# Performance work log

Measured on AMD Instinct MI355X. Metric: run time of the kernel, lower is better.

Reference implementation:

```python
import jax, jax.numpy as jnp
import numpy as np

N_TBINS = 1024
K = 8
B = 32768
IRF_SIGMA = 10.0
PEAK_FACTOR = 5.0
# IRF1DLayer: circular pad (pad_l=N//2, pad_r=N//2-1 for even N) then conv1d with
# flip(irf)  ==  circular convolution with irf followed by roll of -(N-1-N//2).
ROLL_C = N_TBINS - 1 - N_TBINS // 2  # 511


def _wrapped_gaussian(n, mu, sigma):
    # circ_shifted gaussian pulse: wrap tails around the domain, normalize to unit area
    t = np.arange(n, dtype=np.float64)
    g = np.zeros(n, dtype=np.float64)
    for s in (-n, 0, n):
        g += np.exp(-((t - mu + s) ** 2) / (2.0 * sigma ** 2))
    g /= g.sum()
    return jnp.asarray(g, dtype=jnp.float32)


def _circ_conv(x, irf):
    # faithful IRF1DLayer: circular convolution, recentered
    y = jnp.fft.irfft(jnp.fft.rfft(x, axis=-1) * jnp.fft.rfft(irf), n=N_TBINS, axis=-1)
    return jnp.roll(y, -ROLL_C, axis=-1)


def setup_inputs():
    key = jax.random.key(0)
    k1, k2, k3, k4 = jax.random.split(key, 4)
    illumination = _wrapped_gaussian(N_TBINS, N_TBINS // 2, 30.0)  # Gaussian1DLayer buffer
    irf = _wrapped_gaussian(N_TBINS, (N_TBINS - 1) // 2, IRF_SIGMA)
    photon_counts = jax.random.uniform(k1, (B,), jnp.float32, 10.0, 1000.0)
    sbrs = jax.random.uniform(k2, (B,), jnp.float32, 0.1, 1.0)
    bins = jax.random.randint(k3, (B,), 0, N_TBINS)
    cmat_weight = jax.random.normal(k4, (K, N_TBINS), jnp.float32) * 0.05  # Conv1d(k, n_tbins, 1) weight
    return {"illumination": illumination, "photon_counts": photon_counts,
            "sbrs": sbrs, "irf": irf, "cmat_weight": cmat_weight, "bins": bins}


def reference(illumination, photon_counts, sbrs, irf, cmat_weight, bins):
    n = N_TBINS
    inp = _circ_conv(jax.nn.relu(illumination), irf)          # [N] = irf(relu(illum))
    shifts = (bins % n).astype(jnp.int32)                     # [B]
    amb_per_bin = (photon_counts / sbrs) / n                  # [B]
    area = jnp.sum(inp)                                       # current_area
    scale = photon_counts / area                              # [B]
    scaled = inp[None, :] * scale[:, None]                    # [B, N]
    clamped = jnp.minimum(scaled, (PEAK_FACTOR * photon_counts)[:, None])
    offset = clamped + amb_per_bin[:, None]                   # [B, N]
    conv = _circ_conv(offset, irf)                            # [B, N] (batched FFT conv)
    # torch.roll(x, s): out[t] = x[(t - s) % N], vectorized over batch
    idx = (jnp.arange(n)[None, :] - shifts[:, None]) % n      # [B, N]
    shifted = jnp.take_along_axis(conv, idx, axis=1)          # [B, N]
    rate = jax.lax.stop_gradient(shifted)                     # torch.poisson detaches
    noisy = jax.random.poisson(jax.random.key(42), rate, shape=rate.shape).astype(jnp.float32)
    # cmat1D: Conv1d(in=n_tbins, out=k, kernel=1) on [B, N, 1] -> [B, K, 1]
    out = jnp.einsum('bn,kn->bk', noisy, cmat_weight)[..., None]
    return out
```

## Files before the change

kernel.cpp:

```cpp
#include <hip/hip_runtime.h>
#include <hip/hip_bf16.h>
#include <stdint.h>

#define N_T   1024
#define ROLLC 511
#define KCH   8
#define KN_LEV 48
#define DENSE_L 3
#define RJ_LEV 24
#define CH_N  (2*KN_LEV + 4*RJ_LEV)

__device__ double   g_inp[N_T];
__device__ double   g_conv2[N_T];
__device__ double   g_area;
__device__ uint32_t g_chains[CH_N];
__device__ int      g_T;
__device__ float    g_ll5, g_aa5, g_bb5, g_inva5, g_vr5;

struct TF2 { uint32_t x, y; };

__device__ __forceinline__ TF2 tf2x32(uint32_t k0, uint32_t k1, uint32_t c0, uint32_t c1) {
  uint32_t ks2 = k0 ^ k1 ^ 0x1BD11BDAu;
  uint32_t x0 = c0 + k0, x1 = c1 + k1;
#define TFR(r) { x0 += x1; x1 = (x1 << (r)) | (x1 >> (32 - (r))); x1 ^= x0; }
  TFR(13) TFR(15) TFR(26) TFR(6)
  x0 += k1;  x1 += ks2 + 1u;
  TFR(17) TFR(29) TFR(16) TFR(24)
  x0 += ks2; x1 += k0 + 2u;
  TFR(13) TFR(15) TFR(26) TFR(6)
  x0 += k0;  x1 += k1 + 3u;
  TFR(17) TFR(29) TFR(16) TFR(24)
  x0 += k1;  x1 += ks2 + 4u;
  TFR(13) TFR(15) TFR(26) TFR(6)
  x0 += ks2; x1 += k0 + 5u;
#undef TFR
  return {x0, x1};
}

__device__ __forceinline__ float u01_from_key(uint32_t sk0, uint32_t sk1, uint32_t m) {
  TF2 r = tf2x32(sk0, sk1, 0u, m);
  uint32_t bits = r.x ^ r.y;
  return __uint_as_float((bits >> 9) | 0x3f800000u) - 1.0f;
}

__device__ __forceinline__ float lgamma_xla(float x) {
#pragma clang fp contract(off)
  float z = x - 1.0f;
  float sum = 1.0f;
  sum = sum + 676.5203681218851f     / (z + 1.0f);
  sum = sum + -1259.1392167224028f   / (z + 2.0f);
  sum = sum + 771.32342877765313f    / (z + 3.0f);
  sum = sum + -176.61502916214059f   / (z + 4.0f);
  sum = sum + 12.507343278686905f    / (z + 5.0f);
  sum = sum + -0.13857109526572012f  / (z + 6.0f);
  sum = sum + 9.9843695780195716e-6f / (z + 7.0f);
  sum = sum + 1.5056327351493116e-7f / (z + 8.0f);
  float t = 7.5f + z;
  float log_t = 2.0149030205422647f + log1pf(z / 7.5f);
  return 0.91893853320467274f + (z + 0.5f - t / log_t) * log_t + logf(sum);
}

__device__ __forceinline__ void rej_constants(float lam, float* ll, float* aa, float* bb,
                                              float* inva, float* vr) {
#pragma clang fp contract(off)
  *ll = logf(lam);
  float b = 0.931f + 2.53f * sqrtf(lam);
  float a = -0.059f + 0.02483f * b;
  *bb = b; *aa = a;
  *inva = 1.1239f + 1.1328f / (b - 3.4f);
  *vr = 0.9277f - 3.6224f / (b - 2.0f);
}

__device__ __forceinline__ int ptrs_quick(float lamr, float aa, float bb, float vr,
                                          float u, float v) {
#pragma clang fp contract(off)
  float us = 0.5f - fabsf(u);
  float kf = floorf((2.0f * aa / us + bb) * u + lamr + 0.43f);
  if ((us >= 0.07f) && (v <= vr)) return 1;
  if ((kf < 0.0f) || ((us < 0.013f) && (v > us))) return -1;
  return 0;
}

__device__ __forceinline__ bool ptrs_slow(float lamr, float ll, float aa, float bb,
                                          float inva, float u, float v) {
#pragma clang fp contract(off)
  float us = 0.5f - fabsf(u);
  float kf = floorf((2.0f * aa / us + bb) * u + lamr + 0.43f);
  float s = logf(v * inva / (aa / (us * us) + bb));
  float t = (-lamr + kf * ll) - lgamma_xla(kf + 1.0f);
  return s <= t;
}

__device__ __forceinline__ bool rej_iter(float lam, float ll, float aa, float bb,
                                         float inva, float vr, float u, float v, float* kf) {
#pragma clang fp contract(off)
  float us = 0.5f - fabsf(u);
  float k = floorf((2.0f * aa / us + bb) * u + lam + 0.43f);
  *kf = k;
  if ((us >= 0.07f) && (v <= vr)) return true;
  if ((k < 0.0f) || ((us < 0.013f) && (v > us))) return false;
  float s = logf(v * inva / (aa / (us * us) + bb));
  float t = (-lam + k * ll) - lgamma_xla(k + 1.0f);
  return s <= t;
}

__device__ __forceinline__ uint32_t wave_append(bool pred, uint32_t* counter) {
  unsigned long long vote = __ballot(pred);
  int lane = threadIdx.x & 63;
  uint32_t base = 0;
  int cnt = __popcll(vote);
  if (cnt) {
    int leader = __ffsll((unsigned long long)vote) - 1;
    if (lane == leader) base = atomicAdd(counter, (uint32_t)cnt);
    base = (uint32_t)__shfl((int)base, leader, 64);
  }
  return base + (uint32_t)__popcll(vote & ((1ull << lane) - 1ull));
}

__global__ void __launch_bounds__(128)
pre1_kernel(const float* __restrict__ illum, const float* __restrict__ irf) {
  __shared__ double xs[N_T], irfs[N_T];
  const int tid = threadIdx.x;
  for (int i = tid; i < N_T; i += 128) {
    xs[i]   = fmax((double)illum[i], 0.0);
    irfs[i] = (double)irf[i];
  }
  __syncthreads();
  const int t  = blockIdx.x * 128 + tid;
  const int tt = (t + ROLLC) & (N_T - 1);
  double acc = 0.0;
  for (int j = 0; j < N_T; ++j) acc += xs[j] * irfs[(tt - j) & (N_T - 1)];
  g_inp[t] = acc;
}

__global__ void __launch_bounds__(128)
pre2_kernel(const float* __restrict__ irf, uint32_t* __restrict__ wcount) {
  __shared__ double inps[N_T], irfs[N_T];
  const int tid = threadIdx.x;
  if (blockIdx.x < 8) {
    for (int i = tid; i < N_T; i += 128) {
      inps[i] = g_inp[i];
      irfs[i] = (double)irf[i];
    }
    __syncthreads();
    const int t  = blockIdx.x * 128 + tid;
    const int tt = (t + ROLLC) & (N_T - 1);
    double acc = 0.0;
    for (int j = 0; j < N_T; ++j) acc += inps[j] * irfs[(tt - j) & (N_T - 1)];
    g_conv2[t] = acc;
  } else {
    if (tid == 0) {
      g_T = 1;
      wcount[0] = 0u;
      double area = 0.0;
      for (int j = 0; j < N_T; ++j) area += g_inp[j];
      g_area = area;
    } else if (tid == 1) {
      uint32_t r0 = 0u, r1 = 42u;
      for (int j = 0; j < KN_LEV; ++j) {
        TF2 sub = tf2x32(r0, r1, 0u, 1u);
        TF2 nxt = tf2x32(r0, r1, 0u, 0u);
        g_chains[2*j] = sub.x; g_chains[2*j+1] = sub.y;
        r0 = nxt.x; r1 = nxt.y;
      }
    } else if (tid == 2) {
      uint32_t c0 = 0u, c1 = 42u;
      for (int j = 0; j < RJ_LEV; ++j) {
        TF2 nxt = tf2x32(c0, c1, 0u, 0u);
        TF2 s0  = tf2x32(c0, c1, 0u, 1u);
        TF2 s1  = tf2x32(c0, c1, 0u, 2u);
        int base = 2*KN_LEV + 4*j;
        g_chains[base]   = s0.x; g_chains[base+1] = s0.y;
        g_chains[base+2] = s1.x; g_chains[base+3] = s1.y;
        c0 = nxt.x; c1 = nxt.y;
      }
    } else if (tid == 3) {
      float ll, aa, bb, inva, vr;
      rej_constants(1e5f, &ll, &aa, &bb, &inva, &vr);
      g_ll5 = ll; g_aa5 = aa; g_bb5 = bb; g_inva5 = inva; g_vr5 = vr;
    }
  }
}

__global__ void __launch_bounds__(256)
t1_kernel(const float* __restrict__ photon, const float* __restrict__ sbr,
          const int* __restrict__ bins, uint32_t* __restrict__ wcount,
          uint2* __restrict__ recs, uint32_t cap) {
  __shared__ uint2    lrec[N_T];
  __shared__ uint32_t amb_m[N_T];
  __shared__ float    amb_u[N_T], amb_v[N_T], amb_lam[N_T];
  __shared__ uint32_t lcount, acount, gbase;
  const int b = blockIdx.x, tid = threadIdx.x;
  if (tid == 0) { lcount = 0u; acount = 0u; }
  __syncthreads();

  const float ph = photon[b], sb = sbr[b];
  const int   shift = bins[b] & (N_T - 1);
  const double scale = (double)ph / g_area;
  const float  r1f = ph / sb;
  const double amb = (double)r1f * (1.0 / 1024.0);
  const uint32_t sa0 = g_chains[2*KN_LEV+0], sa1 = g_chains[2*KN_LEV+1];
  const uint32_t sc0 = g_chains[2*KN_LEV+2], sc1 = g_chains[2*KN_LEV+3];
  const float ll5 = g_ll5, aa5 = g_aa5, bb5 = g_bb5, inva5 = g_inva5, vr5 = g_vr5;
  const uint32_t mbase = (uint32_t)b << 10;

  for (int i2 = 0; i2 < 4; ++i2) {
    const int t   = tid + (i2 << 8);
    const int src = (t - shift) & (N_T - 1);
    const float lam = (float)(scale * g_conv2[src] + amb);
    float lamr, aa, bbv, vr;
    if (lam < 10.0f) { lamr = 1e5f; aa = aa5; bbv = bb5; vr = vr5; }
    else {
#pragma clang fp contract(off)
      lamr = lam;
      float b2 = 0.931f + 2.53f * sqrtf(lam);
      bbv = b2; aa = -0.059f + 0.02483f * b2;
      vr = 0.9277f - 3.6224f / (b2 - 2.0f);
    }
    const uint32_t m = mbase + (uint32_t)t;
    float u = u01_from_key(sa0, sa1, m) - 0.5f;
    float v = u01_from_key(sc0, sc1, m);
    int cls = ptrs_quick(lamr, aa, bbv, vr, u, v);
    bool surv = (cls < 0);
    bool ambg = (cls == 0);
    uint32_t sS = wave_append(surv, &lcount);
    if (surv) lrec[sS] = make_uint2(m, __float_as_uint(lamr));
    uint32_t sA = wave_append(ambg, &acount);
    if (ambg) { amb_m[sA] = m; amb_u[sA] = u; amb_v[sA] = v; amb_lam[sA] = lamr; }
  }
  __syncthreads();

  const uint32_t na = acount;
  const uint32_t naPad = (na + 255u) & ~255u;
  for (uint32_t i = tid; i < naPad; i += 256) {
    bool active = (i < na);
    bool surv = false;
    uint32_t m = 0; float lamr = 0.f;
    if (active) {
      m = amb_m[i]; lamr = amb_lam[i];
      float u = amb_u[i], v = amb_v[i];
      float ll, aa, bbv, inva;
      if (lamr == 1e5f) { ll = ll5; aa = aa5; bbv = bb5; inva = inva5; }
      else {
#pragma clang fp contract(off)
        float b2 = 0.931f + 2.53f * sqrtf(lamr);
        bbv = b2; aa = -0.059f + 0.02483f * b2;
        ll = logf(lamr);
        inva = 1.1239f + 1.1328f / (b2 - 3.4f);
      }
      surv = !ptrs_slow(lamr, ll, aa, bbv, inva, u, v);
    }
    uint32_t sS = wave_append(surv, &lcount);
    if (surv) lrec[sS] = make_uint2(m, __float_as_uint(lamr));
  }
  __syncthreads();

  if (tid == 0) gbase = atomicAdd(wcount, lcount);
  __syncthreads();
  const uint32_t lc = lcount, base = gbase;
  for (uint32_t i = tid; i < lc; i += 256) {
    const uint32_t g = base + i;
    uint2 r = lrec[i];
    if (g < cap) {
      recs[g] = r;
    } else {
      const uint32_t m = r.x; const float lamr = __uint_as_float(r.y);
      float ll, aaf, bbf, invaf, vrf;
      if (lamr == 1e5f) { ll = ll5; aaf = aa5; bbf = bb5; invaf = inva5; vrf = vr5; }
      else rej_constants(lamr, &ll, &aaf, &bbf, &invaf, &vrf);
      int jf = RJ_LEV;
#pragma unroll 1
      for (int j = 1; j < RJ_LEV; ++j) {
        const uint32_t* c = g_chains + 2*KN_LEV + 4*j;
        float uu = u01_from_key(c[0], c[1], m) - 0.5f;
        float vv = u01_from_key(c[2], c[3], m);
        float kk;
        if (rej_iter(lamr, ll, aaf, bbf, invaf, vrf, uu, vv, &kk)) { jf = j + 1; break; }
      }
      atomicMax(&g_T, jf);
    }
  }
}

__global__ void __launch_bounds__(256)
t2_kernel(const uint32_t* __restrict__ wcount, const uint2* __restrict__ recs, uint32_t cap) {
  __shared__ uint32_t chs[4*RJ_LEV];
  __shared__ int bmax;
  const int tid = threadIdx.x;
  if (tid < 4*RJ_LEV) chs[tid] = g_chains[2*KN_LEV + tid];
  if (tid == 0) bmax = 1;
  __syncthreads();
  uint32_t n = *wcount; if (n > cap) n = cap;
  const float ll5 = g_ll5, aa5 = g_aa5, bb5 = g_bb5, inva5 = g_inva5, vr5 = g_vr5;
  int mymax = 1;
  for (uint32_t gi = blockIdx.x * 256u + tid; gi < n; gi += gridDim.x * 256u) {
    uint2 r = recs[gi];
    const uint32_t m = r.x; const float lamr = __uint_as_float(r.y);
    float ll, aa, bbv, inva, vr;
    if (lamr == 1e5f) { ll = ll5; aa = aa5; bbv = bb5; inva = inva5; vr = vr5; }
    else rej_constants(lamr, &ll, &aa, &bbv, &inva, &vr);
    int jf = RJ_LEV;
#pragma unroll 1
    for (int j = 1; j < RJ_LEV; ++j) {
      float uu = u01_from_key(chs[4*j], chs[4*j+1], m) - 0.5f;
      float vv = u01_from_key(chs[4*j+2], chs[4*j+3], m);
      float kk;
      if (rej_iter(lamr, ll, aa, bbv, inva, vr, uu, vv, &kk)) { jf = j + 1; break; }
    }
    mymax = max(mymax, jf);
  }
  for (int off = 32; off > 0; off >>= 1) mymax = max(mymax, __shfl_down(mymax, off, 64));
  if ((tid & 63) == 0) atomicMax(&bmax, mymax);
  __syncthreads();
  if (tid == 0) atomicMax(&g_T, bmax);
}

__global__ void __launch_bounds__(256)
sample_kernel(const float* __restrict__ photon, const float* __restrict__ sbr,
              const int* __restrict__ bins, const float* __restrict__ w,
              float* __restrict__ out) {
  __shared__ uint32_t ch[CH_N];
  __shared__ float lamS[N_T];
  __shared__ float cntS[N_T];
  __shared__ uint16_t rejL[N_T];
  __shared__ uint16_t surPK[N_T];
  __shared__ float    surLP[N_T];
  __shared__ uint32_t nSur, nRej;
  __shared__ float wred[4][KCH];
  const int b = blockIdx.x, tid = threadIdx.x;
  if (tid < CH_N) ch[tid] = g_chains[tid];
  if (tid == 0) { nSur = 0u; nRej = 0u; }
  __syncthreads();

  const float ph = photon[b], sb = sbr[b];
  const int   shift = bins[b] & (N_T - 1);
  const double scale = (double)ph / g_area;
  const float  r1f = ph / sb;
  const double amb = (double)r1f * (1.0 / 1024.0);
  const uint32_t mbase = (uint32_t)b << 10;

  for (int i2 = 0; i2 < 4; ++i2) {
    const int t   = tid + (i2 << 8);
    const int src = (t - shift) & (N_T - 1);
    const float lam = (float)(scale * g_conv2[src] + amb);
    lamS[t] = lam;
    const bool kn = (lam < 10.0f);
    const float neg = -lam;
    const uint32_t m = mbase + (uint32_t)t;
    float lp = 0.0f; int k = 0;
#pragma unroll
    for (int j = 0; j < DENSE_L; ++j) {
      k += (lp > neg) ? 1 : 0;
      float u = u01_from_key(ch[2*j], ch[2*j+1], m);
      lp += __logf(u);
    }
    const bool alive = (lp > neg);
    if (kn && !alive) cntS[t] = (float)(k - 1);
    bool srv = kn && alive;
    uint32_t sS = wave_append(srv, &nSur);
    if (srv) { surPK[sS] = (uint16_t)((k << 10) | t); surLP[sS] = lp; }
    uint32_t sR = wave_append(!kn, &nRej);
    if (!kn) rejL[sR] = (uint16_t)t;
  }
  __syncthreads();

  {
    const uint32_t nS = nSur;
    for (uint32_t i = tid; i < nS; i += 256) {
      const uint16_t pk = surPK[i];
      const uint16_t t16 = pk & 1023u;
      int k = pk >> 10;
      float lp = surLP[i];
      const float neg = -lamS[t16];
      const uint32_t m = mbase + (uint32_t)t16;
      int j = DENSE_L;
#pragma unroll 1
      while ((lp > neg) && (j < KN_LEV)) {
        ++k;
        lp += __logf(u01_from_key(ch[2*j], ch[2*j+1], m));
        ++j;
      }
      cntS[t16] = (float)(k - 1);
    }
  }

  {
    const int T = g_T;
    const uint32_t nr = nRej;
    for (uint32_t i = tid; i < nr; i += 256) {
      const uint16_t t16 = rejL[i];
      const float lam = lamS[t16];
      const uint32_t m = mbase + (uint32_t)t16;
      float ll, aa, bbv, inva, vr;
      rej_constants(lam, &ll, &aa, &bbv, &inva, &vr);
      float kout = -1.0f;
#pragma unroll 1
      for (int j = T - 1; j >= 0; --j) {
        const uint32_t* c = ch + 2*KN_LEV + 4*j;
        float u = u01_from_key(c[0], c[1], m) - 0.5f;
        float v = u01_from_key(c[2], c[3], m);
        float kf;
        if (rej_iter(lam, ll, aa, bbv, inva, vr, u, v, &kf)) { kout = kf; break; }
      }
      cntS[t16] = kout;
    }
  }
  __syncthreads();

  float acc[KCH];
#pragma unroll
  for (int k = 0; k < KCH; ++k) acc[k] = 0.0f;
  for (int i2 = 0; i2 < 4; ++i2) {
    const int t = tid + (i2 << 8);
    const float c = cntS[t];
#pragma unroll
    for (int k = 0; k < KCH; ++k) acc[k] += c * w[k * N_T + t];
  }
  const int lane = tid & 63, wv = tid >> 6;
#pragma unroll
  for (int k = 0; k < KCH; ++k) {
    float v = acc[k];
    for (int off = 32; off > 0; off >>= 1) v += __shfl_down(v, off, 64);
    if (lane == 0) wred[wv][k] = v;
  }
  __syncthreads();
  if (tid < KCH)
    out[b * KCH + tid] = wred[0][tid] + wred[1][tid] + wred[2][tid] + wred[3][tid];
}

extern "C" void kernel_launch(void* const* d_in, const int* in_sizes, int n_in,
                              void* d_out, int out_size, void* d_ws, size_t ws_size,
                              hipStream_t stream) {
  (void)n_in; (void)out_size;
  const float* illum  = (const float*)d_in[0];
  const float* photon = (const float*)d_in[1];
  const float* sbr    = (const float*)d_in[2];
  const float* irf    = (const float*)d_in[3];
  const float* w      = (const float*)d_in[4];
  const int*   bins   = (const int*)d_in[5];
  float* out = (float*)d_out;
  const int B = in_sizes[1];

  uint32_t* wcount = (uint32_t*)d_ws;
  uint2*    recs   = (uint2*)((char*)d_ws + 16);
  uint32_t  cap    = (ws_size > 16) ? (uint32_t)((ws_size - 16) / sizeof(uint2)) : 0u;

  pre1_kernel<<<8, 128, 0, stream>>>(illum, irf);
  pre2_kernel<<<9, 128, 0, stream>>>(irf, wcount);
  t1_kernel<<<B, 256, 0, stream>>>(photon, sbr, bins, wcount, recs, cap);
  t2_kernel<<<2048, 256, 0, stream>>>(wcount, recs, cap);
  sample_kernel<<<B, 256, 0, stream>>>(photon, sbr, bins, w, out);
}
```

Baseline: 1.137 ms.

## Fuse Knuth Poisson sampling into first pass and slim rejection-only second pass

The Knuth small-lambda sampling and its partial dot products move into the first per-batch kernel, which also does the PTRS quick/slow classification. The ambiguous slow test now runs inline instead of through a separate compaction pass. Shared-memory append counters are replaced with per-wave register counters and wave-local staging, and the dense Knuth depth is sized adaptively from the wave's maximum lambda. The final kernel only handles rejection-sampled bins, with the loop unrolled by four, and atomically adds to the output, returning early when a block has none. This removes one full pass over lambda and several block barriers, at the cost of more divergence and more register pressure in the fused kernel.

```diff
diff --git a/kernel.cpp b/kernel.cpp
--- a/kernel.cpp
+++ b/kernel.cpp
@@ -6,7 +6,6 @@
 #define ROLLC 511
 #define KCH   8
 #define KN_LEV 48
-#define DENSE_L 3
 #define RJ_LEV 24
 #define CH_N  (2*KN_LEV + 4*RJ_LEV)
 
@@ -102,19 +101,6 @@
   float s = logf(v * inva / (aa / (us * us) + bb));
   float t = (-lam + k * ll) - lgamma_xla(k + 1.0f);
   return s <= t;
-}
-
-__device__ __forceinline__ uint32_t wave_append(bool pred, uint32_t* counter) {
-  unsigned long long vote = __ballot(pred);
-  int lane = threadIdx.x & 63;
-  uint32_t base = 0;
-  int cnt = __popcll(vote);
-  if (cnt) {
-    int leader = __ffsll((unsigned long long)vote) - 1;
-    if (lane == leader) base = atomicAdd(counter, (uint32_t)cnt);
-    base = (uint32_t)__shfl((int)base, leader, 64);
-  }
-  return base + (uint32_t)__popcll(vote & ((1ull << lane) - 1ull));
 }
 
 __global__ void __launch_bounds__(128)
@@ -183,84 +169,146 @@
 }
 
 __global__ void __launch_bounds__(256)
-t1_kernel(const float* __restrict__ photon, const float* __restrict__ sbr,
-          const int* __restrict__ bins, uint32_t* __restrict__ wcount,
+kA_kernel(const float* __restrict__ photon, const float* __restrict__ sbr,
+          const int* __restrict__ bins, const float* __restrict__ w,
+          float* __restrict__ out, uint32_t* __restrict__ wcount,
           uint2* __restrict__ recs, uint32_t cap) {
-  __shared__ uint2    lrec[N_T];
-  __shared__ uint32_t amb_m[N_T];
-  __shared__ float    amb_u[N_T], amb_v[N_T], amb_lam[N_T];
-  __shared__ uint32_t lcount, acount, gbase;
+  __shared__ uint32_t ch[CH_N];
+  __shared__ uint2    sstage[N_T];
+  __shared__ uint16_t tpk[N_T];
+  __shared__ float    tlp[N_T];
+  __shared__ uint32_t scnts[4];
+  __shared__ uint32_t sbase;
+  __shared__ float    wred[4][KCH];
   const int b = blockIdx.x, tid = threadIdx.x;
-  if (tid == 0) { lcount = 0u; acount = 0u; }
-  __syncthreads();
-
-  const float ph = photon[b], sb = sbr[b];
-  const int   shift = bins[b] & (N_T - 1);
+  const int wv = tid >> 6, lane = tid & 63;
+  for (int i = tid; i < CH_N; i += 256) ch[i] = g_chains[i];
+  __syncthreads();
+
+  const float  ph = photon[b], sb = sbr[b];
+  const int    shift = bins[b] & (N_T - 1);
   const double scale = (double)ph / g_area;
   const float  r1f = ph / sb;
   const double amb = (double)r1f * (1.0 / 1024.0);
-  const uint32_t sa0 = g_chains[2*KN_LEV+0], sa1 = g_chains[2*KN_LEV+1];
-  const uint32_t sc0 = g_chains[2*KN_LEV+2], sc1 = g_chains[2*KN_LEV+3];
+  const uint32_t mbase = (uint32_t)b << 10;
+  const uint32_t ka0 = ch[2*KN_LEV+0], ka1 = ch[2*KN_LEV+1];
+  const uint32_t kc0 = ch[2*KN_LEV+2], kc1 = ch[2*KN_LEV+3];
   const float ll5 = g_ll5, aa5 = g_aa5, bb5 = g_bb5, inva5 = g_inva5, vr5 = g_vr5;
-  const uint32_t mbase = (uint32_t)b << 10;
+  const unsigned long long lmask = (1ull << lane) - 1ull;
+
+  uint32_t wcS = 0;
+  uint32_t wcT = 0;
+  float acc[KCH];
+#pragma unroll
+  for (int k = 0; k < KCH; ++k) acc[k] = 0.0f;
 
   for (int i2 = 0; i2 < 4; ++i2) {
-    const int t   = tid + (i2 << 8);
+    const int t   = (wv << 8) + (i2 << 6) + lane;
     const int src = (t - shift) & (N_T - 1);
     const float lam = (float)(scale * g_conv2[src] + amb);
-    float lamr, aa, bbv, vr;
-    if (lam < 10.0f) { lamr = 1e5f; aa = aa5; bbv = bb5; vr = vr5; }
-    else {
-#pragma clang fp contract(off)
-      lamr = lam;
-      float b2 = 0.931f + 2.53f * sqrtf(lam);
-      bbv = b2; aa = -0.059f + 0.02483f * b2;
-      vr = 0.9277f - 3.6224f / (b2 - 2.0f);
-    }
-    const uint32_t m = mbase + (uint32_t)t;
-    float u = u01_from_key(sa0, sa1, m) - 0.5f;
-    float v = u01_from_key(sc0, sc1, m);
-    int cls = ptrs_quick(lamr, aa, bbv, vr, u, v);
-    bool surv = (cls < 0);
-    bool ambg = (cls == 0);
-    uint32_t sS = wave_append(surv, &lcount);
-    if (surv) lrec[sS] = make_uint2(m, __float_as_uint(lamr));
-    uint32_t sA = wave_append(ambg, &acount);
-    if (ambg) { amb_m[sA] = m; amb_u[sA] = u; amb_v[sA] = v; amb_lam[sA] = lamr; }
-  }
-  __syncthreads();
-
-  const uint32_t na = acount;
-  const uint32_t naPad = (na + 255u) & ~255u;
-  for (uint32_t i = tid; i < naPad; i += 256) {
-    bool active = (i < na);
-    bool surv = false;
-    uint32_t m = 0; float lamr = 0.f;
-    if (active) {
-      m = amb_m[i]; lamr = amb_lam[i];
-      float u = amb_u[i], v = amb_v[i];
-      float ll, aa, bbv, inva;
-      if (lamr == 1e5f) { ll = ll5; aa = aa5; bbv = bb5; inva = inva5; }
-      else {
-#pragma clang fp contract(off)
-        float b2 = 0.931f + 2.53f * sqrtf(lamr);
-        bbv = b2; aa = -0.059f + 0.02483f * b2;
-        ll = logf(lamr);
-        inva = 1.1239f + 1.1328f / (b2 - 3.4f);
+    const bool  isRej = (lam >= 10.0f);
+    const float lamr  = isRej ? lam : 1e5f;
+    const uint32_t m  = mbase + (uint32_t)t;
+
+    float u = u01_from_key(ka0, ka1, m) - 0.5f;
+    float v = u01_from_key(kc0, kc1, m);
+    float bbq, aaq, vrq;
+    {
+#pragma clang fp contract(off)
+      float b2 = 0.931f + 2.53f * sqrtf(lamr);
+      float aq = -0.059f + 0.02483f * b2;
+      float vq = 0.9277f - 3.6224f / (b2 - 2.0f);
+      bbq = isRej ? b2 : bb5;
+      aaq = isRej ? aq : aa5;
+      vrq = isRej ? vq : vr5;
+    }
+    int cls = ptrs_quick(lamr, aaq, bbq, vrq, u, v);
+    bool surv;
+    if (cls == 0) {
+      float ll   = isRej ? logf(lamr) : ll5;
+      float inva;
+      {
+#pragma clang fp contract(off)
+        inva = isRej ? (1.1239f + 1.1328f / (bbq - 3.4f)) : inva5;
       }
-      surv = !ptrs_slow(lamr, ll, aa, bbv, inva, u, v);
-    }
-    uint32_t sS = wave_append(surv, &lcount);
-    if (surv) lrec[sS] = make_uint2(m, __float_as_uint(lamr));
-  }
-  __syncthreads();
-
-  if (tid == 0) gbase = atomicAdd(wcount, lcount);
-  __syncthreads();
-  const uint32_t lc = lcount, base = gbase;
-  for (uint32_t i = tid; i < lc; i += 256) {
+      surv = !ptrs_slow(lamr, ll, aaq, bbq, inva, u, v);
+    } else {
+      surv = (cls < 0);
+    }
+    {
+      unsigned long long vote = __ballot(surv);
+      uint32_t slot = wcS + (uint32_t)__popcll(vote & lmask);
+      if (surv) sstage[(wv << 8) + slot] = make_uint2(m, __float_as_uint(lamr));
+      wcS += (uint32_t)__popcll(vote);
+    }
+
+    const bool kn = !isRej;
+    const float neg = kn ? -lam : 1.0f;
+    float glam = kn ? lam : 0.0f;
+#pragma unroll
+    for (int off = 32; off > 0; off >>= 1) glam = fmaxf(glam, __shfl_xor(glam, off, 64));
+    int D = 0;
+    if (glam > 0.0f) {
+      D = (int)(glam + 2.0f * sqrtf(glam)) + 2;
+      if (D > KN_LEV) D = KN_LEV;
+    }
+    float lp = 0.0f; int k = 0;
+    for (int j = 0; j < D; ++j) {
+      k += (lp > neg) ? 1 : 0;
+      lp += __logf(u01_from_key(ch[2*j], ch[2*j+1], m));
+    }
+    const bool alive = kn && (lp > neg);
+    const float cntf = (kn && !alive) ? (float)(k - 1) : 0.0f;
+#pragma unroll
+    for (int kk = 0; kk < KCH; ++kk) acc[kk] += cntf * w[kk * N_T + t];
+    {
+      unsigned long long vote = __ballot(alive);
+      uint32_t slot = wcT + (uint32_t)__popcll(vote & lmask);
+      if (alive) { tpk[(wv << 8) + slot] = (uint16_t)(((uint32_t)k << 10) | (uint32_t)t);
+                   tlp[(wv << 8) + slot] = lp; }
+      wcT += (uint32_t)__popcll(vote);
+    }
+  }
+
+  for (uint32_t i = lane; i < wcT; i += 64) {
+    const uint32_t pk = tpk[(wv << 8) + i];
+    const uint32_t t  = pk & 1023u;
+    int k = (int)(pk >> 10);
+    float lp = tlp[(wv << 8) + i];
+    const int src = ((int)t - shift) & (N_T - 1);
+    const float lam = (float)(scale * g_conv2[src] + amb);
+    const float neg = -lam;
+    const uint32_t m = mbase + t;
+    int j = k;
+#pragma unroll 1
+    while ((lp > neg) && (j < KN_LEV)) {
+      ++k;
+      lp += __logf(u01_from_key(ch[2*j], ch[2*j+1], m));
+      ++j;
+    }
+    const float cntf = (float)(k - 1);
+#pragma unroll
+    for (int kk = 0; kk < KCH; ++kk) acc[kk] += cntf * w[kk * N_T + t];
+  }
+
+#pragma unroll
+  for (int kk = 0; kk < KCH; ++kk) {
+    float vv = acc[kk];
+    for (int off = 32; off > 0; off >>= 1) vv += __shfl_down(vv, off, 64);
+    if (lane == 0) wred[wv][kk] = vv;
+  }
+  if (lane == 0) scnts[wv] = wcS;
+  __syncthreads();
+  if (tid == 0) sbase = atomicAdd(wcount, scnts[0] + scnts[1] + scnts[2] + scnts[3]);
+  if (tid < KCH)
+    out[b * KCH + tid] = wred[0][tid] + wred[1][tid] + wred[2][tid] + wred[3][tid];
+  __syncthreads();
+  uint32_t pre = 0;
+  for (int ww = 0; ww < wv; ++ww) pre += scnts[ww];
+  const uint32_t base = sbase + pre;
+  for (uint32_t i = lane; i < wcS; i += 64) {
     const uint32_t g = base + i;
-    uint2 r = lrec[i];
+    const uint2 r = sstage[(wv << 8) + i];
     if (g < cap) {
       recs[g] = r;
     } else {
@@ -271,9 +319,8 @@
       int jf = RJ_LEV;
 #pragma unroll 1
       for (int j = 1; j < RJ_LEV; ++j) {
-        const uint32_t* c = g_chains + 2*KN_LEV + 4*j;
-        float uu = u01_from_key(c[0], c[1], m) - 0.5f;
-        float vv = u01_from_key(c[2], c[3], m);
+        float uu = u01_from_key(ch[2*KN_LEV + 4*j], ch[2*KN_LEV + 4*j + 1], m) - 0.5f;
+        float vv = u01_from_key(ch[2*KN_LEV + 4*j + 2], ch[2*KN_LEV + 4*j + 3], m);
         float kk;
         if (rej_iter(lamr, ll, aaf, bbf, invaf, vrf, uu, vv, &kk)) { jf = j + 1; break; }
       }
@@ -316,116 +363,89 @@
 }
 
 __global__ void __launch_bounds__(256)
-sample_kernel(const float* __restrict__ photon, const float* __restrict__ sbr,
-              const int* __restrict__ bins, const float* __restrict__ w,
-              float* __restrict__ out) {
-  __shared__ uint32_t ch[CH_N];
-  __shared__ float lamS[N_T];
-  __shared__ float cntS[N_T];
-  __shared__ uint16_t rejL[N_T];
-  __shared__ uint16_t surPK[N_T];
-  __shared__ float    surLP[N_T];
-  __shared__ uint32_t nSur, nRej;
+kB_kernel(const float* __restrict__ photon, const float* __restrict__ sbr,
+          const int* __restrict__ bins, const float* __restrict__ w,
+          float* __restrict__ out) {
+  __shared__ int haveRej;
   __shared__ float wred[4][KCH];
   const int b = blockIdx.x, tid = threadIdx.x;
-  if (tid < CH_N) ch[tid] = g_chains[tid];
-  if (tid == 0) { nSur = 0u; nRej = 0u; }
-  __syncthreads();
-
-  const float ph = photon[b], sb = sbr[b];
-  const int   shift = bins[b] & (N_T - 1);
+  const int wv = tid >> 6, lane = tid & 63;
+  if (tid == 0) haveRej = 0;
+  __syncthreads();
+  const float  ph = photon[b], sb = sbr[b];
+  const int    shift = bins[b] & (N_T - 1);
   const double scale = (double)ph / g_area;
   const float  r1f = ph / sb;
   const double amb = (double)r1f * (1.0 / 1024.0);
   const uint32_t mbase = (uint32_t)b << 10;
+  const int T = g_T;
+
+  float acc[KCH];
+#pragma unroll
+  for (int k = 0; k < KCH; ++k) acc[k] = 0.0f;
+  bool any = false;
 
   for (int i2 = 0; i2 < 4; ++i2) {
-    const int t   = tid + (i2 << 8);
+    const int t   = (wv << 8) + (i2 << 6) + lane;
     const int src = (t - shift) & (N_T - 1);
     const float lam = (float)(scale * g_conv2[src] + amb);
-    lamS[t] = lam;
-    const bool kn = (lam < 10.0f);
-    const float neg = -lam;
-    const uint32_t m = mbase + (uint32_t)t;
-    float lp = 0.0f; int k = 0;
-#pragma unroll
-    for (int j = 0; j < DENSE_L; ++j) {
-      k += (lp > neg) ? 1 : 0;
-      float u = u01_from_key(ch[2*j], ch[2*j+1], m);
-      lp += __logf(u);
-    }
-    const bool alive = (lp > neg);
-    if (kn && !alive) cntS[t] = (float)(k - 1);
-    bool srv = kn && alive;
-    uint32_t sS = wave_append(srv, &nSur);
-    if (srv) { surPK[sS] = (uint16_t)((k << 10) | t); surLP[sS] = lp; }
-    uint32_t sR = wave_append(!kn, &nRej);
-    if (!kn) rejL[sR] = (uint16_t)t;
-  }
-  __syncthreads();
-
-  {
-    const uint32_t nS = nSur;
-    for (uint32_t i = tid; i < nS; i += 256) {
-      const uint16_t pk = surPK[i];
-      const uint16_t t16 = pk & 1023u;
-      int k = pk >> 10;
-      float lp = surLP[i];
-      const float neg = -lamS[t16];
-      const uint32_t m = mbase + (uint32_t)t16;
-      int j = DENSE_L;
-#pragma unroll 1
-      while ((lp > neg) && (j < KN_LEV)) {
-        ++k;
-        lp += __logf(u01_from_key(ch[2*j], ch[2*j+1], m));
-        ++j;
-      }
-      cntS[t16] = (float)(k - 1);
-    }
-  }
-
-  {
-    const int T = g_T;
-    const uint32_t nr = nRej;
-    for (uint32_t i = tid; i < nr; i += 256) {
-      const uint16_t t16 = rejL[i];
-      const float lam = lamS[t16];
-      const uint32_t m = mbase + (uint32_t)t16;
+    if (lam >= 10.0f) {
+      any = true;
+      const uint32_t m = mbase + (uint32_t)t;
       float ll, aa, bbv, inva, vr;
       rej_constants(lam, &ll, &aa, &bbv, &inva, &vr);
       float kout = -1.0f;
+      bool found = false;
 #pragma unroll 1
-      for (int j = T - 1; j >= 0; --j) {
-        const uint32_t* c = ch + 2*KN_LEV + 4*j;
-        float u = u01_from_key(c[0], c[1], m) - 0.5f;
-        float v = u01_from_key(c[2], c[3], m);
-        float kf;
-        if (rej_iter(lam, ll, aa, bbv, inva, vr, u, v, &kf)) { kout = kf; break; }
+      for (int jj = T - 1; jj >= 0 && !found; jj -= 4) {
+        float kf0, kf1, kf2, kf3;
+        bool a0 = false, a1 = false, a2 = false, a3 = false;
+        {
+          const uint32_t* c = g_chains + 2*KN_LEV + 4*jj;
+          a0 = rej_iter(lam, ll, aa, bbv, inva, vr,
+                        u01_from_key(c[0], c[1], m) - 0.5f,
+                        u01_from_key(c[2], c[3], m), &kf0);
+        }
+        if (jj - 1 >= 0) {
+          const uint32_t* c = g_chains + 2*KN_LEV + 4*(jj-1);
+          a1 = rej_iter(lam, ll, aa, bbv, inva, vr,
+                        u01_from_key(c[0], c[1], m) - 0.5f,
+                        u01_from_key(c[2], c[3], m), &kf1);
+        }
+        if (jj - 2 >= 0) {
+          const uint32_t* c = g_chains + 2*KN_LEV + 4*(jj-2);
+          a2 = rej_iter(lam, ll, aa, bbv, inva, vr,
+                        u01_from_key(c[0], c[1], m) - 0.5f,
+                        u01_from_key(c[2], c[3], m), &kf2);
+        }
+        if (jj - 3 >= 0) {
+          const uint32_t* c = g_chains + 2*KN_LEV + 4*(jj-3);
+          a3 = rej_iter(lam, ll, aa, bbv, inva, vr,
+                        u01_from_key(c[0], c[1], m) - 0.5f,
+                        u01_from_key(c[2], c[3], m), &kf3);
+        }
+        if      (a0) { kout = kf0; found = true; }
+        else if (a1) { kout = kf1; found = true; }
+        else if (a2) { kout = kf2; found = true; }
+        else if (a3) { kout = kf3; found = true; }
       }
-      cntS[t16] = kout;
-    }
-  }
-  __syncthreads();
-
-  float acc[KCH];
-#pragma unroll
-  for (int k = 0; k < KCH; ++k) acc[k] = 0.0f;
-  for (int i2 = 0; i2 < 4; ++i2) {
-    const int t = tid + (i2 << 8);
-    const float c = cntS[t];
-#pragma unroll
-    for (int k = 0; k < KCH; ++k) acc[k] += c * w[k * N_T + t];
-  }
-  const int lane = tid & 63, wv = tid >> 6;
-#pragma unroll
-  for (int k = 0; k < KCH; ++k) {
-    float v = acc[k];
-    for (int off = 32; off > 0; off >>= 1) v += __shfl_down(v, off, 64);
-    if (lane == 0) wred[wv][k] = v;
+#pragma unroll
+      for (int kk = 0; kk < KCH; ++kk) acc[kk] += kout * w[kk * N_T + t];
+    }
+  }
+
+  if (any) haveRej = 1;
+  __syncthreads();
+  if (!haveRej) return;
+#pragma unroll
+  for (int kk = 0; kk < KCH; ++kk) {
+    float vv = acc[kk];
+    for (int off = 32; off > 0; off >>= 1) vv += __shfl_down(vv, off, 64);
+    if (lane == 0) wred[wv][kk] = vv;
   }
   __syncthreads();
   if (tid < KCH)
-    out[b * KCH + tid] = wred[0][tid] + wred[1][tid] + wred[2][tid] + wred[3][tid];
+    atomicAdd(&out[b * KCH + tid], wred[0][tid] + wred[1][tid] + wred[2][tid] + wred[3][tid]);
 }
 
 extern "C" void kernel_launch(void* const* d_in, const int* in_sizes, int n_in,
@@ -447,7 +467,7 @@
 
   pre1_kernel<<<8, 128, 0, stream>>>(illum, irf);
   pre2_kernel<<<9, 128, 0, stream>>>(irf, wcount);
-  t1_kernel<<<B, 256, 0, stream>>>(photon, sbr, bins, wcount, recs, cap);
+  kA_kernel<<<B, 256, 0, stream>>>(photon, sbr, bins, w, out, wcount, recs, cap);
   t2_kernel<<<2048, 256, 0, stream>>>(wcount, recs, cap);
-  sample_kernel<<<B, 256, 0, stream>>>(photon, sbr, bins, w, out);
-}
+  kB_kernel<<<B, 256, 0, stream>>>(photon, sbr, bins, w, out);
+}
```

Measured after the change: 1.316 ms. 1.16x slower.

## Compact Poisson survivor lists across rounds of three levels to reduce divergence

Applied to the files above, without the earlier changes.

The per-thread open-ended loop over surviving small-lambda Poisson elements is replaced by block-wide rounds. Each round advances every survivor by up to three product-of-uniforms levels, then compacts the ones still alive into a ping-pong shared list for the next round. The aim is to keep waves densely occupied instead of idling behind the few long-running lanes. In exchange it adds block barriers and atomic appends every round, plus a second set of shared lists.

```diff
diff --git a/kernel.cpp b/kernel.cpp
--- a/kernel.cpp
+++ b/kernel.cpp
@@ -323,13 +323,13 @@
   __shared__ float lamS[N_T];
   __shared__ float cntS[N_T];
   __shared__ uint16_t rejL[N_T];
-  __shared__ uint16_t surPK[N_T];
-  __shared__ float    surLP[N_T];
-  __shared__ uint32_t nSur, nRej;
+  __shared__ uint16_t listA[N_T], listB[N_T];
+  __shared__ float    lpA[N_T], lpB[N_T];
+  __shared__ uint32_t nA, nB, nRej;
   __shared__ float wred[4][KCH];
   const int b = blockIdx.x, tid = threadIdx.x;
   if (tid < CH_N) ch[tid] = g_chains[tid];
-  if (tid == 0) { nSur = 0u; nRej = 0u; }
+  if (tid == 0) { nA = 0u; nB = 0u; nRej = 0u; }
   __syncthreads();
 
   const float ph = photon[b], sb = sbr[b];
@@ -357,32 +357,51 @@
     const bool alive = (lp > neg);
     if (kn && !alive) cntS[t] = (float)(k - 1);
     bool srv = kn && alive;
-    uint32_t sS = wave_append(srv, &nSur);
-    if (srv) { surPK[sS] = (uint16_t)((k << 10) | t); surLP[sS] = lp; }
+    uint32_t sS = wave_append(srv, &nA);
+    if (srv) { listA[sS] = (uint16_t)t; lpA[sS] = lp; }
     uint32_t sR = wave_append(!kn, &nRej);
     if (!kn) rejL[sR] = (uint16_t)t;
   }
-  __syncthreads();
 
   {
-    const uint32_t nS = nSur;
-    for (uint32_t i = tid; i < nS; i += 256) {
-      const uint16_t pk = surPK[i];
-      const uint16_t t16 = pk & 1023u;
-      int k = pk >> 10;
-      float lp = surLP[i];
-      const float neg = -lamS[t16];
-      const uint32_t m = mbase + (uint32_t)t16;
-      int j = DENSE_L;
+    uint16_t* cur = listA;  float* clp = lpA;  uint32_t* curn = &nA;
+    uint16_t* nxt = listB;  float* nlp = lpB;  uint32_t* nxtn = &nB;
+    int jstart = DENSE_L;
+    while (true) {
+      __syncthreads();
+      const uint32_t nn = *curn;
+      if (nn == 0u) break;
+      if (jstart >= KN_LEV) {
+        for (uint32_t i = tid; i < nn; i += 256) cntS[cur[i]] = (float)(KN_LEV - 1);
+        break;
+      }
+      if (tid == 0) *nxtn = 0u;
+      __syncthreads();
+      const int L = (jstart + 3 <= KN_LEV) ? 3 : (KN_LEV - jstart);
+      const uint32_t nnPad = (nn + 255u) & ~255u;
+      for (uint32_t i = tid; i < nnPad; i += 256) {
+        const bool active = (i < nn);
+        uint16_t t16 = 0; float lp = 0.0f, neg = 1.0f;
+        if (active) { t16 = cur[i]; lp = clp[i]; neg = -lamS[t16]; }
+        const uint32_t m = mbase + (uint32_t)t16;
+        int p = 0;
 #pragma unroll 1
-      while ((lp > neg) && (j < KN_LEV)) {
-        ++k;
-        lp += __logf(u01_from_key(ch[2*j], ch[2*j+1], m));
-        ++j;
-      }
-      cntS[t16] = (float)(k - 1);
-    }
-  }
+        for (int s = 0; s < L; ++s) {
+          p += (lp > neg) ? 1 : 0;
+          lp += __logf(u01_from_key(ch[2*(jstart+s)], ch[2*(jstart+s)+1], m));
+        }
+        const bool alive = active && (p == L);
+        if (active && !alive) cntS[t16] = (float)(jstart + p - 1);
+        uint32_t slot = wave_append(alive, nxtn);
+        if (alive) { nxt[slot] = t16; nlp[slot] = lp; }
+      }
+      { uint16_t* tp = cur; cur = nxt; nxt = tp; }
+      { float* tp = clp; clp = nlp; nlp = tp; }
+      { uint32_t* tp = curn; curn = nxtn; nxtn = tp; }
+      jstart += L;
+    }
+  }
+  __syncthreads();
 
   {
     const int T = g_T;
```

New measurement: 1.262 ms. 1.11x slower.
